# Kernel optimization log

Hardware: AMD Instinct MI355X
Metric: run time of the kernel (lower is better)

## Reference

```python
import jax, jax.numpy as jnp
import numpy as np
import math

D_MODEL = 512
N_TOTAL = 1024
HW = 4096
EPSILON = 0.2
NUM_HEADS = 8
D_K = D_MODEL // NUM_HEADS
BATCH = 4


def setup_inputs() -> dict:
    rng = jax.random.key(0)
    ks = jax.random.split(rng, 16)
    s = 1.0 / math.sqrt(D_MODEL)
    inp = {
        "query": jax.random.normal(ks[0], (BATCH, N_TOTAL, D_MODEL), jnp.float32),
        "key": jax.random.normal(ks[1], (BATCH, HW, D_MODEL), jnp.float32),
        "value": jax.random.normal(ks[2], (BATCH, HW, D_MODEL), jnp.float32),
        "x_tilde": jax.random.uniform(ks[3], (HW, 2), jnp.float32),
        "x_hat": jax.random.uniform(ks[4], (N_TOTAL, HW, 2), jnp.float32),
        # torch nn.Linear params: W is (out, in), y = x @ W.T + b
        "Wq": jax.random.uniform(ks[5], (D_MODEL, D_MODEL), jnp.float32, -s, s),
        "bq": jax.random.uniform(ks[6], (D_MODEL,), jnp.float32, -s, s),
        "Wk": jax.random.uniform(ks[7], (D_MODEL, D_MODEL), jnp.float32, -s, s),
        "bk": jax.random.uniform(ks[8], (D_MODEL,), jnp.float32, -s, s),
        "Wv": jax.random.uniform(ks[9], (D_MODEL, D_MODEL), jnp.float32, -s, s),
        "bv": jax.random.uniform(ks[10], (D_MODEL,), jnp.float32, -s, s),
        "Wo": jax.random.uniform(ks[11], (D_MODEL, D_MODEL), jnp.float32, -s, s),
        "bo": jax.random.uniform(ks[12], (D_MODEL,), jnp.float32, -s, s),
    }
    return inp


def _geo_mask(x_tilde, x_hat):
    # x_tilde: (HW, 2), x_hat: (N_total, HW, 2)
    diff = x_tilde[None, :, :] - x_hat            # (N, HW, 2)
    dist = jnp.sqrt(jnp.sum(diff * diff, axis=-1))  # (N, HW)
    return jnp.where(dist < EPSILON, 0.0, -jnp.inf).astype(x_hat.dtype)


def reference(query, key, value, x_tilde, x_hat, Wq, bq, Wk, bk, Wv, bv, Wo, bo):
    B = query.shape[0]
    M_geo = _geo_mask(x_tilde, x_hat)  # (N, HW)

    def heads(x, W, b):
        y = x @ W.T + b                                   # (B, L, D)
        return y.reshape(B, -1, NUM_HEADS, D_K).transpose(0, 2, 1, 3)  # (B, H, L, dk)

    Q = heads(query, Wq, bq)   # (B, H, N, dk)
    K = heads(key, Wk, bk)     # (B, H, HW, dk)
    V = heads(value, Wv, bv)   # (B, H, HW, dk)

    scores = jnp.einsum("bhnd,bhmd->bhnm", Q, K) / math.sqrt(D_K)
    scores = scores + M_geo[None, None, :, :]
    attn = jax.nn.softmax(scores, axis=-1)                # (B, H, N, HW)
    ctx = jnp.einsum("bhnm,bhmd->bhnd", attn, V)          # (B, H, N, dk)
    ctx = ctx.transpose(0, 2, 1, 3).reshape(B, -1, D_MODEL)
    out = ctx @ Wo.T + bo                                 # (B, N, D)
    return out, attn
```

## Files before the change

### kernel.cpp

```cpp
#include <hip/hip_runtime.h>
#include <cstdint>
#include <cstddef>

typedef __attribute__((ext_vector_type(4))) float f32x4;
typedef __attribute__((ext_vector_type(8))) short s16x8;
typedef __attribute__((ext_vector_type(4))) short s16x4;
typedef unsigned short u16;
typedef unsigned long long u64;

static __device__ inline u16 f2bf(float f) {
    unsigned u = __builtin_bit_cast(unsigned, f);
    u += 0x7fffu + ((u >> 16) & 1u);
    return (u16)(u >> 16);
}

static __device__ inline f32x4 mfma16(s16x8 a, s16x8 b, f32x4 c) {
    return __builtin_amdgcn_mfma_f32_16x16x32_bf16(a, b, c, 0, 0, 0);
}

static __device__ inline float redsum16(float v) {
    v += __shfl_xor(v, 1);
    v += __shfl_xor(v, 2);
    v += __shfl_xor(v, 4);
    v += __shfl_xor(v, 8);
    return v;
}

__global__ __launch_bounds__(256) void cvt_bf16_kernel(const float* __restrict__ src,
                                                       u16* __restrict__ dst, float scale) {
    int i = (blockIdx.x * 256 + threadIdx.x) * 4;
    f32x4 v = *(const f32x4*)(src + i);
    s16x4 o;
    o[0] = (short)f2bf(v[0] * scale); o[1] = (short)f2bf(v[1] * scale);
    o[2] = (short)f2bf(v[2] * scale); o[3] = (short)f2bf(v[3] * scale);
    *(s16x4*)(dst + i) = o;
}

__global__ __launch_bounds__(256) void mask_kernel(const float* __restrict__ xt,
                                                   const float* __restrict__ xh,
                                                   u64* __restrict__ mb) {
    int tid  = threadIdx.x;
    int lane = tid & 63;
    int wv   = blockIdx.x * 4 + (tid >> 6);
    int n    = wv >> 6;
    int mbk  = wv & 63;
    int m    = (mbk << 6) + lane;
    size_t hidx = ((size_t)n * 4096 + m) * 2;
    float dx = xt[2 * m]     - xh[hidx];
    float dy = xt[2 * m + 1] - xh[hidx + 1];
    bool p = sqrtf(dx * dx + dy * dy) < 0.2f;
    u64 bal = __ballot(p);
    if (lane == 0) mb[wv] = bal;
}

template <int INF32, int MODE, int LSHIFT>
__global__ __launch_bounds__(256) void proj_kernel(const void* __restrict__ Xv,
                                                   const u16* __restrict__ Wb,
                                                   const float* __restrict__ bias,
                                                   float bscale,
                                                   void* __restrict__ Yv) {
    __shared__ u16 aT[128 * 72];
    __shared__ u16 bT[128 * 72];

    int tid  = threadIdx.x;
    int lane = tid & 63, w = tid >> 6, q = lane >> 4, m15 = lane & 15;
    int wm = w >> 1, wn = w & 1;
    int m0 = blockIdx.x * 128, n0 = blockIdx.y * 128;
    int sRow = tid >> 1, sC = (tid & 1) * 32;

    f32x4 acc[4][4];
#pragma unroll
    for (int i = 0; i < 4; ++i)
#pragma unroll
        for (int j = 0; j < 4; ++j) { f32x4 z = {0.f, 0.f, 0.f, 0.f}; acc[i][j] = z; }

    for (int kb = 0; kb < 512; kb += 64) {
        if (INF32) {
            const float* X = (const float*)Xv;
#pragma unroll
            for (int j = 0; j < 8; ++j) {
                int col = sC + j * 4;
                f32x4 v = *(const f32x4*)(X + (size_t)(m0 + sRow) * 512 + kb + col);
                s16x4 o;
                o[0] = (short)f2bf(v[0]); o[1] = (short)f2bf(v[1]);
                o[2] = (short)f2bf(v[2]); o[3] = (short)f2bf(v[3]);
                *(s16x4*)(aT + sRow * 72 + col) = o;
            }
        } else {
            const u16* X = (const u16*)Xv;
#pragma unroll
            for (int j = 0; j < 4; ++j) {
                int col = sC + j * 8;
                s16x8 v = *(const s16x8*)(X + (size_t)(m0 + sRow) * 512 + kb + col);
                *(s16x8*)(aT + sRow * 72 + col) = v;
            }
        }
#pragma unroll
        for (int j = 0; j < 4; ++j) {
            int col = sC + j * 8;
            s16x8 v = *(const s16x8*)(Wb + (size_t)(n0 + sRow) * 512 + kb + col);
            *(s16x8*)(bT + sRow * 72 + col) = v;
        }
        __syncthreads();
#pragma unroll
        for (int kk = 0; kk < 2; ++kk) {
            s16x8 af[4], bf[4];
#pragma unroll
            for (int t = 0; t < 4; ++t) {
                af[t] = *(const s16x8*)(aT + (wm * 64 + t * 16 + m15) * 72 + kk * 32 + q * 8);
                bf[t] = *(const s16x8*)(bT + (wn * 64 + t * 16 + m15) * 72 + kk * 32 + q * 8);
            }
#pragma unroll
            for (int am = 0; am < 4; ++am)
#pragma unroll
                for (int bn = 0; bn < 4; ++bn)
                    acc[am][bn] = mfma16(af[am], bf[bn], acc[am][bn]);
        }
        __syncthreads();
    }

#pragma unroll
    for (int am = 0; am < 4; ++am) {
        int mg = m0 + wm * 64 + am * 16 + q * 4;
#pragma unroll
        for (int bn = 0; bn < 4; ++bn) {
            int col = n0 + wn * 64 + bn * 16 + m15;
            float bv = bias[col] * bscale;
            if (MODE == 2) {
                float* Y = (float*)Yv;
#pragma unroll
                for (int r = 0; r < 4; ++r)
                    Y[(size_t)(mg + r) * 512 + col] = acc[am][bn][r] + bv;
            } else if (MODE == 3) {
                u16* Y = (u16*)Yv;
                int hh = col >> 6, d = col & 63;
#pragma unroll
                for (int r = 0; r < 4; ++r) {
                    int m = mg + r;
                    int bb = m >> LSHIFT;
                    int nn = m & ((1 << LSHIFT) - 1);
                    Y[(((size_t)(bb * 8 + hh) << LSHIFT) + nn) * 64 + d] = f2bf(acc[am][bn][r] + bv);
                }
            } else {
                u16* Yt = (u16*)Yv;
                int bidx = mg >> 12, hw0 = mg & 4095;
                int hh = col >> 6, d = col & 63;
                s16x4 o;
#pragma unroll
                for (int r = 0; r < 4; ++r) o[r] = (short)f2bf(acc[am][bn][r] + bv);
                *(s16x4*)(Yt + ((size_t)((bidx << 3) + hh) * 64 + d) * 4096 + hw0) = o;
            }
        }
    }
}

__global__ __launch_bounds__(512) void attn_kernel(const u16* __restrict__ Qh,
                                                   const u16* __restrict__ Kh,
                                                   const u16* __restrict__ Vt,
                                                   const u64* __restrict__ mbits,
                                                   float* __restrict__ attnO,
                                                   u16* __restrict__ ctxO) {
    __shared__ u64   smask[2048];
    __shared__ float sred[8][32];
    __shared__ float srowi[32];
    __shared__ u16   sps[8][2][16 * 72];
    __shared__ float sctx[2048];

    int tid  = threadIdx.x;
    int lane = tid & 63, w = tid >> 6, q = lane >> 4, m15 = lane & 15;
    int i = blockIdx.x;
    int jj = i >> 3;
    int bh = (i & 7) * 4 + (jj & 3);
    int n0 = (jj >> 2) * 32;
    int b = bh >> 3, h = bh & 7;

    for (int t = tid; t < 2048; t += 512) {
        smask[t] = mbits[(size_t)n0 * 64 + t];
        sctx[t]  = 0.f;
    }
    __syncthreads();

    s16x8 aQ[2][2];
#pragma unroll
    for (int g = 0; g < 2; ++g) {
        const u16* Qp = Qh + (((size_t)bh << 10) + n0 + g * 16 + m15) * 64 + q * 8;
        aQ[g][0] = *(const s16x8*)(Qp);
        aQ[g][1] = *(const s16x8*)(Qp + 32);
    }

    const u16* Kp = Kh + (((size_t)bh << 12) + (w << 9) + m15) * 64 + q * 8;
    const float L2E = 1.44269504f;

    float ls[2][4] = {{0.f,0.f,0.f,0.f},{0.f,0.f,0.f,0.f}};
    for (int t4 = 0; t4 < 8; ++t4) {
        int widx = w * 8 + t4;
        u64 mk[2][4];
#pragma unroll
        for (int g = 0; g < 2; ++g)
#pragma unroll
            for (int r = 0; r < 4; ++r) mk[g][r] = smask[(g * 16 + q * 4 + r) * 64 + widx];
#pragma unroll
        for (int tt = 0; tt < 4; ++tt) {
            const u16* kp = Kp + (size_t)(t4 * 4 + tt) * (16 * 64);
            s16x8 b0 = *(const s16x8*)(kp);
            s16x8 b1 = *(const s16x8*)(kp + 32);
            f32x4 z = {0.f, 0.f, 0.f, 0.f};
            f32x4 c0 = mfma16(aQ[0][0], b0, mfma16(aQ[0][1], b1, z));
            f32x4 c1 = mfma16(aQ[1][0], b0, mfma16(aQ[1][1], b1, z));
            int bit = tt * 16 + m15;
#pragma unroll
            for (int r = 0; r < 4; ++r) {
                float p0 = ((mk[0][r] >> bit) & 1ull) ? exp2f(c0[r] * L2E) : 0.f;
                float p1 = ((mk[1][r] >> bit) & 1ull) ? exp2f(c1[r] * L2E) : 0.f;
                ls[0][r] += p0;
                ls[1][r] += p1;
            }
        }
    }
#pragma unroll
    for (int g = 0; g < 2; ++g)
#pragma unroll
        for (int r = 0; r < 4; ++r) {
            float v = redsum16(ls[g][r]);
            if (m15 == 0) sred[w][g * 16 + q * 4 + r] = v;
        }
    __syncthreads();
    if (tid < 32) {
        float ss = 0.f;
#pragma unroll
        for (int ww = 0; ww < 8; ++ww) ss += sred[ww][tid];
        srowi[tid] = 1.0f / ss;
    }
    __syncthreads();
    float iv[2][4];
#pragma unroll
    for (int g = 0; g < 2; ++g)
#pragma unroll
        for (int r = 0; r < 4; ++r) iv[g][r] = srowi[g * 16 + q * 4 + r];

    const u16* Vp = Vt + (((size_t)bh << 6) + m15) * 4096 + (w << 9) + q * 8;
    float* aBp[2];
#pragma unroll
    for (int g = 0; g < 2; ++g)
        aBp[g] = attnO + (((size_t)bh << 10) + n0 + g * 16 + q * 4) * 4096 + (w << 9) + m15;

    f32x4 ctxa[2][4];
#pragma unroll
    for (int g = 0; g < 2; ++g)
#pragma unroll
        for (int dt = 0; dt < 4; ++dt) { f32x4 z = {0.f, 0.f, 0.f, 0.f}; ctxa[g][dt] = z; }

    for (int cc = 0; cc < 8; ++cc) {
        int widx = w * 8 + cc;
        u64 mk[2][4];
#pragma unroll
        for (int g = 0; g < 2; ++g)
#pragma unroll
            for (int r = 0; r < 4; ++r) mk[g][r] = smask[(g * 16 + q * 4 + r) * 64 + widx];

        f32x4 cs[2][4];
#pragma unroll
        for (int tt = 0; tt < 4; ++tt) {
            const u16* kp = Kp + (size_t)(cc * 4 + tt) * (16 * 64);
            s16x8 b0 = *(const s16x8*)(kp);
            s16x8 b1 = *(const s16x8*)(kp + 32);
            f32x4 z = {0.f, 0.f, 0.f, 0.f};
            f32x4 c0 = mfma16(aQ[0][0], b0, mfma16(aQ[0][1], b1, z));
            f32x4 c1 = mfma16(aQ[1][0], b0, mfma16(aQ[1][1], b1, z));
            int bit = tt * 16 + m15;
#pragma unroll
            for (int r = 0; r < 4; ++r) {
                float p0 = ((mk[0][r] >> bit) & 1ull) ? exp2f(c0[r] * L2E) : 0.f;
                float p1 = ((mk[1][r] >> bit) & 1ull) ? exp2f(c1[r] * L2E) : 0.f;
                sps[w][0][(q * 4 + r) * 72 + tt * 16 + m15] = f2bf(p0);
                sps[w][1][(q * 4 + r) * 72 + tt * 16 + m15] = f2bf(p1);
                cs[0][tt][r] = p0 * iv[0][r];
                cs[1][tt][r] = p1 * iv[1][r];
            }
        }
#pragma unroll
        for (int g = 0; g < 2; ++g)
#pragma unroll
            for (int half = 0; half < 2; ++half) {
                s16x8 aP = *(const s16x8*)(&sps[w][g][m15 * 72 + half * 32 + q * 8]);
#pragma unroll
                for (int dt = 0; dt < 4; ++dt) {
                    s16x8 bV = *(const s16x8*)(Vp + (size_t)dt * (16 * 4096) + cc * 64 + half * 32);
                    ctxa[g][dt] = mfma16(aP, bV, ctxa[g][dt]);
                }
            }
#pragma unroll
        for (int g = 0; g < 2; ++g)
#pragma unroll
            for (int tt = 0; tt < 4; ++tt)
#pragma unroll
                for (int r = 0; r < 4; ++r)
                    aBp[g][(size_t)r * 4096 + cc * 64 + tt * 16] = cs[g][tt][r];
    }

#pragma unroll
    for (int g = 0; g < 2; ++g)
#pragma unroll
        for (int dt = 0; dt < 4; ++dt)
#pragma unroll
            for (int r = 0; r < 4; ++r)
                atomicAdd(&sctx[(g * 16 + q * 4 + r) * 64 + dt * 16 + m15],
                          ctxa[g][dt][r] * iv[g][r]);
    __syncthreads();
    for (int t = tid; t < 2048; t += 512) {
        int rr = t >> 6, d = t & 63;
        ctxO[(((size_t)b << 10) + n0 + rr) * 512 + h * 64 + d] = f2bf(sctx[t]);
    }
}

extern "C" void kernel_launch(void* const* d_in, const int* in_sizes, int n_in,
                              void* d_out, int out_size, void* d_ws, size_t ws_size,
                              hipStream_t stream) {
    (void)in_sizes; (void)n_in; (void)out_size; (void)ws_size;
    const float* query = (const float*)d_in[0];
    const float* key   = (const float*)d_in[1];
    const float* value = (const float*)d_in[2];
    const float* x_tilde = (const float*)d_in[3];
    const float* x_hat   = (const float*)d_in[4];
    const float* Wq = (const float*)d_in[5];  const float* bq = (const float*)d_in[6];
    const float* Wk = (const float*)d_in[7];  const float* bk = (const float*)d_in[8];
    const float* Wv = (const float*)d_in[9];  const float* bv = (const float*)d_in[10];
    const float* Wo = (const float*)d_in[11]; const float* bo = (const float*)d_in[12];

    char* ws = (char*)d_ws;
    u16* wq   = (u16*)(ws + 0);
    u16* wk   = (u16*)(ws + 524288);
    u16* wv   = (u16*)(ws + 1048576);
    u16* wo   = (u16*)(ws + 1572864);
    u16* Qh   = (u16*)(ws + 2097152);
    u16* Kh   = (u16*)(ws + 6291456);
    u16* Vtb  = (u16*)(ws + 23068672);
    u16* ctxb = (u16*)(ws + 39845888);
    u64* mbits = (u64*)(ws + 44040192);

    cvt_bf16_kernel<<<256, 256, 0, stream>>>(Wq, wq, 0.125f);
    cvt_bf16_kernel<<<256, 256, 0, stream>>>(Wk, wk, 1.0f);
    cvt_bf16_kernel<<<256, 256, 0, stream>>>(Wv, wv, 1.0f);
    cvt_bf16_kernel<<<256, 256, 0, stream>>>(Wo, wo, 1.0f);
    mask_kernel<<<16384, 256, 0, stream>>>(x_tilde, x_hat, mbits);

    proj_kernel<1, 3, 10><<<dim3(32, 4),  256, 0, stream>>>(query, wq, bq, 0.125f, Qh);
    proj_kernel<1, 3, 12><<<dim3(128, 4), 256, 0, stream>>>(key,   wk, bk, 1.0f,   Kh);
    proj_kernel<1, 1, 12><<<dim3(128, 4), 256, 0, stream>>>(value, wv, bv, 1.0f,   Vtb);

    float* attnO = (float*)d_out + 2097152;
    attn_kernel<<<1024, 512, 0, stream>>>(Qh, Kh, Vtb, mbits, attnO, ctxb);

    proj_kernel<0, 2, 10><<<dim3(32, 4), 256, 0, stream>>>(ctxb, wo, bo, 1.0f, d_out);
}
```

Measured before the change: 921.6 us.

## Cache bf16 probabilities in registers to skip QK recompute; halve attention tile rows

The attention kernel now computes QK^T and the masked exp once, packing the bf16 probabilities into a 64-entry register array. The second pass reuses them for the attention-matrix writes and the PV MFMAs instead of recomputing scores, which removes half the QK MFMA and exp work and the repeated K loads. The row tile drops from 32 to 16 per block, doubling the grid to 2048 blocks. The four weight-conversion launches are merged into one kernel. Attention output is now written from the bf16-rounded probabilities, which lowers its precision, and the large register array may hurt occupancy.

```diff
diff --git a/kernel.cpp b/kernel.cpp
--- a/kernel.cpp
+++ b/kernel.cpp
@@ -6,6 +6,7 @@
 typedef __attribute__((ext_vector_type(8))) short s16x8;
 typedef __attribute__((ext_vector_type(4))) short s16x4;
 typedef unsigned short u16;
+typedef unsigned int u32;
 typedef unsigned long long u64;
 
 static __device__ inline u16 f2bf(float f) {
@@ -26,14 +27,23 @@
     return v;
 }
 
-__global__ __launch_bounds__(256) void cvt_bf16_kernel(const float* __restrict__ src,
-                                                       u16* __restrict__ dst, float scale) {
-    int i = (blockIdx.x * 256 + threadIdx.x) * 4;
-    f32x4 v = *(const f32x4*)(src + i);
+__global__ __launch_bounds__(256) void cvt4_kernel(const float* __restrict__ s0,
+                                                   const float* __restrict__ s1,
+                                                   const float* __restrict__ s2,
+                                                   const float* __restrict__ s3,
+                                                   u16* __restrict__ d0, u16* __restrict__ d1,
+                                                   u16* __restrict__ d2, u16* __restrict__ d3) {
+    int blk = blockIdx.x;
+    int m = blk >> 8;
+    int i = ((blk & 255) * 256 + threadIdx.x) * 4;
+    const float* s = (m == 0) ? s0 : (m == 1) ? s1 : (m == 2) ? s2 : s3;
+    u16* d = (m == 0) ? d0 : (m == 1) ? d1 : (m == 2) ? d2 : d3;
+    float sc = (m == 0) ? 0.125f : 1.0f;
+    f32x4 v = *(const f32x4*)(s + i);
     s16x4 o;
-    o[0] = (short)f2bf(v[0] * scale); o[1] = (short)f2bf(v[1] * scale);
-    o[2] = (short)f2bf(v[2] * scale); o[3] = (short)f2bf(v[3] * scale);
-    *(s16x4*)(dst + i) = o;
+    o[0] = (short)f2bf(v[0] * sc); o[1] = (short)f2bf(v[1] * sc);
+    o[2] = (short)f2bf(v[2] * sc); o[3] = (short)f2bf(v[3] * sc);
+    *(s16x4*)(d + i) = o;
 }
 
 __global__ __launch_bounds__(256) void mask_kernel(const float* __restrict__ xt,
@@ -160,154 +170,121 @@
                                                    const u64* __restrict__ mbits,
                                                    float* __restrict__ attnO,
                                                    u16* __restrict__ ctxO) {
-    __shared__ u64   smask[2048];
-    __shared__ float sred[8][32];
-    __shared__ float srowi[32];
-    __shared__ u16   sps[8][2][16 * 72];
-    __shared__ float sctx[2048];
+    __shared__ u64   smask[1024];
+    __shared__ float sred[8][16];
+    __shared__ float srowi[16];
+    __shared__ u16   sps[8][16 * 36];
+    __shared__ float sctx[1024];
 
     int tid  = threadIdx.x;
     int lane = tid & 63, w = tid >> 6, q = lane >> 4, m15 = lane & 15;
     int i = blockIdx.x;
     int jj = i >> 3;
     int bh = (i & 7) * 4 + (jj & 3);
-    int n0 = (jj >> 2) * 32;
+    int n0 = (jj >> 2) * 16;
     int b = bh >> 3, h = bh & 7;
 
-    for (int t = tid; t < 2048; t += 512) {
+    for (int t = tid; t < 1024; t += 512) {
         smask[t] = mbits[(size_t)n0 * 64 + t];
         sctx[t]  = 0.f;
     }
     __syncthreads();
 
-    s16x8 aQ[2][2];
-#pragma unroll
-    for (int g = 0; g < 2; ++g) {
-        const u16* Qp = Qh + (((size_t)bh << 10) + n0 + g * 16 + m15) * 64 + q * 8;
-        aQ[g][0] = *(const s16x8*)(Qp);
-        aQ[g][1] = *(const s16x8*)(Qp + 32);
-    }
+    const u16* Qp = Qh + (((size_t)bh << 10) + n0 + m15) * 64 + q * 8;
+    s16x8 aQ0 = *(const s16x8*)(Qp);
+    s16x8 aQ1 = *(const s16x8*)(Qp + 32);
 
     const u16* Kp = Kh + (((size_t)bh << 12) + (w << 9) + m15) * 64 + q * 8;
     const float L2E = 1.44269504f;
 
-    float ls[2][4] = {{0.f,0.f,0.f,0.f},{0.f,0.f,0.f,0.f}};
+    u32 Pp[64];
+    float ls[4] = {0.f, 0.f, 0.f, 0.f};
+#pragma unroll
     for (int t4 = 0; t4 < 8; ++t4) {
         int widx = w * 8 + t4;
-        u64 mk[2][4];
-#pragma unroll
-        for (int g = 0; g < 2; ++g)
-#pragma unroll
-            for (int r = 0; r < 4; ++r) mk[g][r] = smask[(g * 16 + q * 4 + r) * 64 + widx];
+        u64 mk[4];
+#pragma unroll
+        for (int r = 0; r < 4; ++r) mk[r] = smask[(q * 4 + r) * 64 + widx];
 #pragma unroll
         for (int tt = 0; tt < 4; ++tt) {
-            const u16* kp = Kp + (size_t)(t4 * 4 + tt) * (16 * 64);
+            int t = t4 * 4 + tt;
+            const u16* kp = Kp + (size_t)t * (16 * 64);
             s16x8 b0 = *(const s16x8*)(kp);
             s16x8 b1 = *(const s16x8*)(kp + 32);
             f32x4 z = {0.f, 0.f, 0.f, 0.f};
-            f32x4 c0 = mfma16(aQ[0][0], b0, mfma16(aQ[0][1], b1, z));
-            f32x4 c1 = mfma16(aQ[1][0], b0, mfma16(aQ[1][1], b1, z));
+            f32x4 c = mfma16(aQ0, b0, mfma16(aQ1, b1, z));
             int bit = tt * 16 + m15;
+            float p[4];
 #pragma unroll
             for (int r = 0; r < 4; ++r) {
-                float p0 = ((mk[0][r] >> bit) & 1ull) ? exp2f(c0[r] * L2E) : 0.f;
-                float p1 = ((mk[1][r] >> bit) & 1ull) ? exp2f(c1[r] * L2E) : 0.f;
-                ls[0][r] += p0;
-                ls[1][r] += p1;
-            }
-        }
-    }
-#pragma unroll
-    for (int g = 0; g < 2; ++g)
-#pragma unroll
-        for (int r = 0; r < 4; ++r) {
-            float v = redsum16(ls[g][r]);
-            if (m15 == 0) sred[w][g * 16 + q * 4 + r] = v;
-        }
+                p[r] = ((mk[r] >> bit) & 1ull) ? exp2f(c[r] * L2E) : 0.f;
+                ls[r] += p[r];
+            }
+            Pp[2 * t]     = (u32)f2bf(p[0]) | ((u32)f2bf(p[1]) << 16);
+            Pp[2 * t + 1] = (u32)f2bf(p[2]) | ((u32)f2bf(p[3]) << 16);
+        }
+    }
+#pragma unroll
+    for (int r = 0; r < 4; ++r) {
+        float v = redsum16(ls[r]);
+        if (m15 == 0) sred[w][q * 4 + r] = v;
+    }
     __syncthreads();
-    if (tid < 32) {
+    if (tid < 16) {
         float ss = 0.f;
 #pragma unroll
         for (int ww = 0; ww < 8; ++ww) ss += sred[ww][tid];
         srowi[tid] = 1.0f / ss;
     }
     __syncthreads();
-    float iv[2][4];
-#pragma unroll
-    for (int g = 0; g < 2; ++g)
-#pragma unroll
-        for (int r = 0; r < 4; ++r) iv[g][r] = srowi[g * 16 + q * 4 + r];
+    float iv[4];
+#pragma unroll
+    for (int r = 0; r < 4; ++r) iv[r] = srowi[q * 4 + r];
 
     const u16* Vp = Vt + (((size_t)bh << 6) + m15) * 4096 + (w << 9) + q * 8;
-    float* aBp[2];
-#pragma unroll
-    for (int g = 0; g < 2; ++g)
-        aBp[g] = attnO + (((size_t)bh << 10) + n0 + g * 16 + q * 4) * 4096 + (w << 9) + m15;
-
-    f32x4 ctxa[2][4];
-#pragma unroll
-    for (int g = 0; g < 2; ++g)
-#pragma unroll
-        for (int dt = 0; dt < 4; ++dt) { f32x4 z = {0.f, 0.f, 0.f, 0.f}; ctxa[g][dt] = z; }
-
-    for (int cc = 0; cc < 8; ++cc) {
-        int widx = w * 8 + cc;
-        u64 mk[2][4];
-#pragma unroll
-        for (int g = 0; g < 2; ++g)
-#pragma unroll
-            for (int r = 0; r < 4; ++r) mk[g][r] = smask[(g * 16 + q * 4 + r) * 64 + widx];
-
-        f32x4 cs[2][4];
-#pragma unroll
-        for (int tt = 0; tt < 4; ++tt) {
-            const u16* kp = Kp + (size_t)(cc * 4 + tt) * (16 * 64);
-            s16x8 b0 = *(const s16x8*)(kp);
-            s16x8 b1 = *(const s16x8*)(kp + 32);
-            f32x4 z = {0.f, 0.f, 0.f, 0.f};
-            f32x4 c0 = mfma16(aQ[0][0], b0, mfma16(aQ[0][1], b1, z));
-            f32x4 c1 = mfma16(aQ[1][0], b0, mfma16(aQ[1][1], b1, z));
-            int bit = tt * 16 + m15;
-#pragma unroll
-            for (int r = 0; r < 4; ++r) {
-                float p0 = ((mk[0][r] >> bit) & 1ull) ? exp2f(c0[r] * L2E) : 0.f;
-                float p1 = ((mk[1][r] >> bit) & 1ull) ? exp2f(c1[r] * L2E) : 0.f;
-                sps[w][0][(q * 4 + r) * 72 + tt * 16 + m15] = f2bf(p0);
-                sps[w][1][(q * 4 + r) * 72 + tt * 16 + m15] = f2bf(p1);
-                cs[0][tt][r] = p0 * iv[0][r];
-                cs[1][tt][r] = p1 * iv[1][r];
-            }
-        }
-#pragma unroll
-        for (int g = 0; g < 2; ++g)
-#pragma unroll
-            for (int half = 0; half < 2; ++half) {
-                s16x8 aP = *(const s16x8*)(&sps[w][g][m15 * 72 + half * 32 + q * 8]);
-#pragma unroll
-                for (int dt = 0; dt < 4; ++dt) {
-                    s16x8 bV = *(const s16x8*)(Vp + (size_t)dt * (16 * 4096) + cc * 64 + half * 32);
-                    ctxa[g][dt] = mfma16(aP, bV, ctxa[g][dt]);
-                }
-            }
-#pragma unroll
-        for (int g = 0; g < 2; ++g)
-#pragma unroll
-            for (int tt = 0; tt < 4; ++tt)
-#pragma unroll
-                for (int r = 0; r < 4; ++r)
-                    aBp[g][(size_t)r * 4096 + cc * 64 + tt * 16] = cs[g][tt][r];
-    }
-
-#pragma unroll
-    for (int g = 0; g < 2; ++g)
-#pragma unroll
-        for (int dt = 0; dt < 4; ++dt)
-#pragma unroll
-            for (int r = 0; r < 4; ++r)
-                atomicAdd(&sctx[(g * 16 + q * 4 + r) * 64 + dt * 16 + m15],
-                          ctxa[g][dt][r] * iv[g][r]);
+    float* aB = attnO + (((size_t)bh << 10) + n0 + q * 4) * 4096 + (w << 9) + m15;
+    u16* psw = &sps[w][0];
+    const u16* psr = psw + m15 * 36 + q * 8;
+
+    f32x4 ctxa[4];
+#pragma unroll
+    for (int dt = 0; dt < 4; ++dt) { f32x4 z = {0.f, 0.f, 0.f, 0.f}; ctxa[dt] = z; }
+
+#pragma unroll
+    for (int cc = 0; cc < 16; ++cc) {
+#pragma unroll
+        for (int s = 0; s < 2; ++s) {
+            int t = 2 * cc + s;
+            u32 w0 = Pp[2 * t], w1 = Pp[2 * t + 1];
+            psw[(q * 4 + 0) * 36 + s * 16 + m15] = (u16)(w0);
+            psw[(q * 4 + 1) * 36 + s * 16 + m15] = (u16)(w0 >> 16);
+            psw[(q * 4 + 2) * 36 + s * 16 + m15] = (u16)(w1);
+            psw[(q * 4 + 3) * 36 + s * 16 + m15] = (u16)(w1 >> 16);
+            float f0 = __builtin_bit_cast(float, (w0 << 16));
+            float f1 = __builtin_bit_cast(float, (w0 & 0xffff0000u));
+            float f2 = __builtin_bit_cast(float, (w1 << 16));
+            float f3 = __builtin_bit_cast(float, (w1 & 0xffff0000u));
+            size_t o = (size_t)cc * 32 + s * 16;
+            aB[o]                    = f0 * iv[0];
+            aB[o + (size_t)1 * 4096] = f1 * iv[1];
+            aB[o + (size_t)2 * 4096] = f2 * iv[2];
+            aB[o + (size_t)3 * 4096] = f3 * iv[3];
+        }
+        s16x8 aP = *(const s16x8*)(psr);
+#pragma unroll
+        for (int dt = 0; dt < 4; ++dt) {
+            s16x8 bV = *(const s16x8*)(Vp + (size_t)dt * (16 * 4096) + cc * 32);
+            ctxa[dt] = mfma16(aP, bV, ctxa[dt]);
+        }
+    }
+
+#pragma unroll
+    for (int dt = 0; dt < 4; ++dt)
+#pragma unroll
+        for (int r = 0; r < 4; ++r)
+            atomicAdd(&sctx[(q * 4 + r) * 64 + dt * 16 + m15], ctxa[dt][r] * iv[r]);
     __syncthreads();
-    for (int t = tid; t < 2048; t += 512) {
+    for (int t = tid; t < 1024; t += 512) {
         int rr = t >> 6, d = t & 63;
         ctxO[(((size_t)b << 10) + n0 + rr) * 512 + h * 64 + d] = f2bf(sctx[t]);
     }
@@ -338,10 +315,7 @@
     u16* ctxb = (u16*)(ws + 39845888);
     u64* mbits = (u64*)(ws + 44040192);
 
-    cvt_bf16_kernel<<<256, 256, 0, stream>>>(Wq, wq, 0.125f);
-    cvt_bf16_kernel<<<256, 256, 0, stream>>>(Wk, wk, 1.0f);
-    cvt_bf16_kernel<<<256, 256, 0, stream>>>(Wv, wv, 1.0f);
-    cvt_bf16_kernel<<<256, 256, 0, stream>>>(Wo, wo, 1.0f);
+    cvt4_kernel<<<1024, 256, 0, stream>>>(Wq, Wk, Wv, Wo, wq, wk, wv, wo);
     mask_kernel<<<16384, 256, 0, stream>>>(x_tilde, x_hat, mbits);
 
     proj_kernel<1, 3, 10><<<dim3(32, 4),  256, 0, stream>>>(query, wq, bq, 0.125f, Qh);
@@ -349,7 +323,7 @@
     proj_kernel<1, 1, 12><<<dim3(128, 4), 256, 0, stream>>>(value, wv, bv, 1.0f,   Vtb);
 
     float* attnO = (float*)d_out + 2097152;
-    attn_kernel<<<1024, 512, 0, stream>>>(Qh, Kh, Vtb, mbits, attnO, ctxb);
+    attn_kernel<<<2048, 512, 0, stream>>>(Qh, Kh, Vtb, mbits, attnO, ctxb);
 
     proj_kernel<0, 2, 10><<<dim3(32, 4), 256, 0, stream>>>(ctxb, wo, bo, 1.0f, d_out);
 }
```

Measured after the change: 1.006 ms. +9.2%, slower.
